# Kernel tuning notes

Hardware: AMD Instinct MI355X
Metric: run time of the kernel (lower is better)

## Reference

```python
import jax, jax.numpy as jnp
import numpy as np

# smoothing constants (from init_kwargs)
KERNEL_SIZE = 20
WINDOW = (-10.0, 10.0)
SIGMA = 4.0
AMPLITUDE = 0.5
N_SMOOTH = 331  # 350 - 20 + 1


def setup_inputs() -> dict:
    key = jax.random.key(0)
    ks = jax.random.split(key, 6)
    W, A, M, D = 4000, 64, 6, 500
    wavelengths = jnp.linspace(0.3, 2.5, W, dtype=jnp.float32)  # um
    grid = jnp.linspace(0.25, 2.6, D, dtype=jnp.float32)        # material wavelength tables
    n_tab = 1.3 + 1.5 * jax.random.uniform(ks[0], (M, D), dtype=jnp.float32)
    k_tab = 0.05 * jax.random.uniform(ks[1], (M, D), dtype=jnp.float32)
    fixed_data = jnp.stack([jnp.broadcast_to(grid, (M, D)), n_tab, k_tab], axis=1)  # [M,3,D]
    refractive_index = 1.5 + 1.5 * jax.random.uniform(ks[2], (350,), dtype=jnp.float32)
    compression_ratio = jnp.ones((1,), jnp.float32)
    thickness_above_unk = 0.05 + 0.2 * jax.random.uniform(ks[3], (10,), dtype=jnp.float32)  # um
    thickness_below_unk = 0.05 + 0.2 * jax.random.uniform(ks[4], (9,), dtype=jnp.float32)   # um
    angle_of_incidences = jnp.linspace(0.0, 60.0, A, dtype=jnp.float32)  # degrees
    # stack order: incoming | 10 above | unknown (index M) | 9 below | outgoing
    md = [0] + [1, 2] * 5 + [M] + [3, 4] * 4 + [3] + [5]
    material_distribution = jnp.array(md, dtype=jnp.int32)  # [22]
    unknown_layer_thickness = jnp.array([500.0], jnp.float32)  # nm
    return dict(refractive_index=refractive_index, compression_ratio=compression_ratio,
                fixed_data=fixed_data, thickness_above_unk=thickness_above_unk,
                thickness_below_unk=thickness_below_unk, wavelengths=wavelengths,
                angle_of_incidences=angle_of_incidences,
                material_distribution=material_distribution, polarization=0,
                unknown_layer_thickness=unknown_layer_thickness)


def reference(refractive_index, compression_ratio, fixed_data, thickness_above_unk,
              thickness_below_unk, wavelengths, angle_of_incidences,
              material_distribution, polarization, unknown_layer_thickness):
    D = fixed_data.shape[2]
    n_repeat = D - N_SMOOTH
    # --- gaussian smoothing of the unknown layer's refractive index (valid conv) ---
    x = jnp.linspace(WINDOW[0], WINDOW[1], KERNEL_SIZE)
    g = AMPLITUDE * jnp.exp(-0.5 * (x / SIGMA) ** 2)
    g = (g / jnp.sum(g)).astype(refractive_index.dtype)
    nk_s = jnp.convolve(refractive_index, g, mode='valid')            # [331]
    nk = jnp.concatenate([nk_s, jnp.full((n_repeat,), nk_s[-1], nk_s.dtype)])  # pad to max_data_dim
    dyn_wl = jnp.linspace(jnp.min(wavelengths), jnp.max(wavelengths), N_SMOOTH)
    dyn_wl = jnp.concatenate([dyn_wl, jnp.full((n_repeat,), dyn_wl[-1], dyn_wl.dtype)])
    # --- interpolate all material n,k tables onto the experimental wavelengths ---
    interp = jax.vmap(lambda xp, fp: jnp.interp(wavelengths, xp, fp))
    n_fixc = interp(fixed_data[:, 0], fixed_data[:, 1]) + 1j * interp(fixed_data[:, 0], fixed_data[:, 2])  # [M,W]
    n_unk = jnp.interp(wavelengths, dyn_wl, nk)[None].astype(n_fixc.dtype)  # unknown layer (k=0)
    n_mat = jnp.concatenate([n_fixc, n_unk], axis=0)                  # [M+1, W]
    n_stack = n_mat[material_distribution]                            # [Lyr, W] complex
    # --- thickness list (unknown in nm -> um, scaled by compression ratio) ---
    d_unk = unknown_layer_thickness / 1000.0 * compression_ratio      # [1]
    d = jnp.concatenate([thickness_above_unk, d_unk, thickness_below_unk])  # [L] = [20]
    # --- coherent TMM, vectorized over (angle, wavelength) ---
    th0 = jnp.deg2rad(angle_of_incidences)                            # [A]
    sin0 = (n_stack[0][None, :] * jnp.sin(th0)[:, None])              # [A,W] (Snell invariant)
    sin_th = sin0[None] / n_stack[:, None, :]                         # [Lyr,A,W]
    cos_th = jnp.sqrt(1.0 - sin_th ** 2)
    kz = 2.0 * jnp.pi * n_stack[:, None, :] * cos_th / wavelengths[None, None, :]
    delta = kz[1:-1] * d[:, None, None].astype(kz.dtype)              # [L,A,W]
    nc = n_stack[:, None, :]
    if polarization == 0:  # s-pol
        f = nc * cos_th                                               # [Lyr,A,W]
        r = (f[:-1] - f[1:]) / (f[:-1] + f[1:])                       # [L+1,A,W]
        t = 2.0 * f[:-1] / (f[:-1] + f[1:])
    else:  # p-pol
        num = nc[1:] * cos_th[:-1]
        den = nc[:-1] * cos_th[1:]
        r = (num - den) / (num + den)
        t = 2.0 * nc[:-1, ] * cos_th[:-1] / (num + den)
    # Mtilde = I_0 * prod_j (P_j @ I_j); 2x2 complex recursion via scan
    m00 = 1.0 / t[0]
    m01 = r[0] / t[0]
    m10 = m01
    m11 = m00

    def step(carry, xs):
        c00, c01, c10, c11 = carry
        dl, rj, tj = xs
        em = jnp.exp(-1j * dl) / tj
        ep = jnp.exp(1j * dl) / tj
        a, b, c, dd = em, rj * em, rj * ep, ep
        return (c00 * a + c01 * c, c00 * b + c01 * dd,
                c10 * a + c11 * c, c10 * b + c11 * dd), None

    (m00, m01, m10, m11), _ = jax.lax.scan(step, (m00, m01, m10, m11), (delta, r[1:], t[1:]))
    rr = m10 / m00
    tt = 1.0 / m00
    R = jnp.abs(rr) ** 2                                              # [A,W]
    if polarization == 0:
        f0 = n_stack[0][None] * cos_th[0]
        ff = n_stack[-1][None] * cos_th[-1]
        T = jnp.abs(tt) ** 2 * jnp.real(ff) / jnp.real(f0)
    else:
        T = (jnp.abs(tt) ** 2 * jnp.real(n_stack[-1][None] * jnp.conj(cos_th[-1]))
             / jnp.real(n_stack[0][None] * jnp.conj(cos_th[0])))
    Aabs = 1.0 - R - T
    return jnp.stack([R, T, Aabs])  # [3, A, W]
```

## Files before the change

kernel.cpp:

```cpp
#include <hip/hip_runtime.h>

#define DEV __device__ __forceinline__
#define RCP(x)  __builtin_amdgcn_rcpf(x)
#define SQRT(x) __builtin_amdgcn_sqrtf(x)

constexpr int W_  = 4000;
constexpr int A_  = 64;
constexpr int D_  = 500;
constexpr int NS_ = 331;
constexpr int KS_ = 20;
constexpr int L_  = 22;
constexpr float PIF = 3.14159265358979323846f;

struct cplx { float re, im; };

DEV cplx cmul(cplx a, cplx b) { return { a.re*b.re - a.im*b.im, a.re*b.im + a.im*b.re }; }
DEV cplx cinv(cplx z) {
  float d = RCP(fmaf(z.re, z.re, z.im * z.im));
  return { z.re * d, -z.im * d };
}

DEV cplx csqrtc(cplx z) {
  float x = z.re, y = z.im;
  float mag = SQRT(fmaf(x, x, y * y));
  float t   = SQRT(0.5f * (mag + fabsf(x)));
  float q   = y * 0.5f * RCP(t);
  bool pos  = (x >= 0.0f);
  float re  = pos ? t : fabsf(q);
  float im  = pos ? q : copysignf(t, y);
  return { re, im };
}

__global__ __launch_bounds__(256) void tmm_fused_kernel(
    const float* __restrict__ ri,
    const float* __restrict__ comp,
    const float* __restrict__ fixed,
    const float* __restrict__ tha,
    const float* __restrict__ thb,
    const float* __restrict__ wl,
    const float* __restrict__ ang,
    const int*   __restrict__ md,
    const float* __restrict__ unk,
    float* __restrict__ out)
{
  __shared__ float  s_grid[D_];
  __shared__ float  s_ri[350];
  __shared__ float  s_g[KS_];
  __shared__ int    s_md[L_];
  __shared__ float  s_d[20];
  __shared__ float  s_mn[4], s_mx[4];
  __shared__ float4 s_f[7 * 256];

  const int tid = threadIdx.x;

  for (int i = tid; i < D_;  i += 256) s_grid[i] = fixed[i];
  for (int i = tid; i < 350; i += 256) s_ri[i]   = ri[i];
  if (tid < KS_) {
    float x  = -10.0f + (float)tid * (20.0f / 19.0f);
    float xs = x * 0.25f;
    s_g[tid] = 0.5f * expf(-0.5f * xs * xs);
  }
  if (tid < L_) s_md[tid] = md[tid];
  if (tid < 20)
    s_d[tid] = (tid < 10) ? tha[tid]
             : (tid == 10 ? unk[0] / 1000.0f * comp[0] : thb[tid - 11]);

  float lmin = 3.4e38f, lmax = -3.4e38f;
  for (int i = tid; i < W_; i += 256) {
    float v = wl[i];
    lmin = fminf(lmin, v); lmax = fmaxf(lmax, v);
  }
  #pragma unroll
  for (int o = 32; o; o >>= 1) {
    lmin = fminf(lmin, __shfl_xor(lmin, o, 64));
    lmax = fmaxf(lmax, __shfl_xor(lmax, o, 64));
  }
  if ((tid & 63) == 0) { s_mn[tid >> 6] = lmin; s_mx[tid >> 6] = lmax; }
  __syncthreads();
  const float wmin = fminf(fminf(s_mn[0], s_mn[1]), fminf(s_mn[2], s_mn[3]));
  const float wmax = fmaxf(fmaxf(s_mx[0], s_mx[1]), fmaxf(s_mx[2], s_mx[3]));

  const int a  = blockIdx.y;
  const int w  = blockIdx.x * 256 + tid;
  const int wc = min(w, W_ - 1);
  const float x = wl[wc];

  int lo = 0, hi = D_;
  while (lo < hi) { int mid = (lo + hi) >> 1; if (s_grid[mid] <= x) lo = mid + 1; else hi = mid; }
  const int i = min(max(lo, 1), D_ - 1);
  const float gx0 = s_grid[i - 1];
  const float fr  = (x - gx0) * RCP(s_grid[i] - gx0);
  const bool lowc  = (x < s_grid[0]);
  const bool highc = (x > s_grid[D_ - 1]);

  #pragma unroll
  for (int m = 0; m < 6; ++m) {
    const float* nptr = fixed + (m * 3 + 1) * D_;
    const float* kptr = fixed + (m * 3 + 2) * D_;
    float nv = fmaf(fr, nptr[i] - nptr[i - 1], nptr[i - 1]);
    float kv = fmaf(fr, kptr[i] - kptr[i - 1], kptr[i - 1]);
    if (lowc)  { nv = nptr[0];      kv = kptr[0]; }
    if (highc) { nv = nptr[D_ - 1]; kv = kptr[D_ - 1]; }
    s_f[m * 256 + tid] = make_float4(nv, kv, 0.0f, 0.0f);
  }

  {
    float gsum = 0.0f;
    #pragma unroll
    for (int k = 0; k < KS_; ++k) gsum += s_g[k];
    const float ginv  = 1.0f / gsum;
    const float stepd = (wmax - wmin) / (float)(NS_ - 1);
    const float istep = RCP(stepd);
    int j = (int)floorf((x - wmin) * istep) + 1;
    j = min(max(j, 1), NS_ - 1);
    const int j0 = j - 1;
    float a0 = 0.0f, a1 = 0.0f;
    #pragma unroll
    for (int k = 0; k < KS_; ++k) {
      const float gk = s_g[KS_ - 1 - k];
      a0 = fmaf(s_ri[j0 + k], gk, a0);
      a1 = fmaf(s_ri[j0 + 1 + k], gk, a1);
    }
    a0 *= ginv; a1 *= ginv;
    const float d0 = fmaf((float)j0, stepd, wmin);
    const float d1 = fmaf((float)j,  stepd, wmin);
    const float f  = fmaf((x - d0) * RCP(d1 - d0), a1 - a0, a0);
    s_f[6 * 256 + tid] = make_float4(f, 0.0f, 0.0f, 0.0f);
  }

  const float th0  = ang[a] * (PIF / 180.0f);
  const float s0   = sinf(th0);
  const float klam = 2.0f * PIF * RCP(x);

  const int md0 = s_md[0];
  const float4 nn0 = s_f[md0 * 256 + tid];
  const cplx sin0 = { nn0.x * s0, nn0.y * s0 };

  #pragma unroll
  for (int m = 0; m < 7; ++m) {
    const float4 nn = s_f[m * 256 + tid];
    const cplx invn = cinv({ nn.x, nn.y });
    const cplx st   = cmul(sin0, invn);
    const cplx st2  = cmul(st, st);
    const cplx ct   = csqrtc({ 1.0f - st2.re, -st2.im });
    const cplx f    = cmul({ nn.x, nn.y }, ct);
    const cplx fi   = cinv(f);
    s_f[m * 256 + tid] = make_float4(f.re, f.im, fi.re, fi.im);
  }

  cplx u   = { 0.0f, 0.0f };
  cplx tac = { 1.0f, 0.0f };
  float4 fdn = s_f[s_md[L_ - 1] * 256 + tid];
  const float fL_re = fdn.x;

  #pragma unroll
  for (int j = L_ - 2; j >= 1; --j) {
    const float4 fj = s_f[s_md[j] * 256 + tid];
    const cplx q   = cmul({ fdn.x, fdn.y }, { fj.z, fj.w });
    const cplx iop = cinv({ 1.0f + q.re, q.im });
    const cplx r   = cmul({ 1.0f - q.re, -q.im }, iop);

    const float cst = klam * s_d[j - 1];
    const float dr = fj.x * cst, di = fj.y * cst;
    const float e2 = __expf(-di);
    float sn, cs;
    __sincosf(dr, &sn, &cs);
    const cplx ph   = { e2 * cs, e2 * sn };
    const cplx beta = cmul(ph, ph);

    const cplx ru  = cmul(r, u);
    const cplx idn = cinv({ 1.0f + ru.re, ru.im });
    tac = cmul(tac, cmul(cmul(iop, ph), idn));
    u = cmul(beta, cmul({ r.re + u.re, r.im + u.im }, idn));

    fdn = fj;
  }

  const float4 f0v = s_f[md0 * 256 + tid];
  const cplx q0   = cmul({ fdn.x, fdn.y }, { f0v.z, f0v.w });
  const cplx iop0 = cinv({ 1.0f + q0.re, q0.im });
  const cplx r0   = cmul({ 1.0f - q0.re, -q0.im }, iop0);
  const cplx ru0  = cmul(r0, u);
  const cplx idn0 = cinv({ 1.0f + ru0.re, ru0.im });
  const cplx rr   = cmul({ r0.re + u.re, r0.im + u.im }, idn0);
  cplx tt = cmul(cmul(iop0, idn0), tac);

  const float SC = 2097152.0f;
  tt.re *= SC; tt.im *= SC;

  const float R = fmaf(rr.re, rr.re, rr.im * rr.im);
  const float T = fmaf(tt.re, tt.re, tt.im * tt.im) * fL_re * RCP(f0v.x);

  if (w < W_) {
    const int o = a * W_ + w;
    out[o]               = R;
    out[A_ * W_ + o]     = T;
    out[2 * A_ * W_ + o] = 1.0f - R - T;
  }
}

extern "C" void kernel_launch(void* const* d_in, const int* in_sizes, int n_in,
                              void* d_out, int out_size, void* d_ws, size_t ws_size,
                              hipStream_t stream) {
  const float* ri    = (const float*)d_in[0];
  const float* comp  = (const float*)d_in[1];
  const float* fixed = (const float*)d_in[2];
  const float* tha   = (const float*)d_in[3];
  const float* thb   = (const float*)d_in[4];
  const float* wl    = (const float*)d_in[5];
  const float* ang   = (const float*)d_in[6];
  const int*   md    = (const int*)d_in[7];
  const float* unk   = (const float*)d_in[9];
  float* out = (float*)d_out;

  dim3 grid(16, A_);
  tmm_fused_kernel<<<grid, 256, 0, stream>>>(ri, comp, fixed, tha, thb, wl,
                                             ang, md, unk, out);
}
```

Before: 97.37 us.

## Split angle-independent material interpolation into a separate precompute kernel

Material interpolation, the Gaussian smoothing of the unknown index and the (n0/n_m)^2 ratio do not depend on angle, so they are moved into a small precompute kernel that runs once per wavelength and writes 7 float4 per wavelength to workspace. The main kernel then reads these values and only scales by sin^2 of the angle, which removes redundant interpolation, binary search and min/max reduction across all 64 angle blocks. The cost is a second launch with a serial dependency and extra global-memory traffic. The per-block shared-memory setup and the __syncthreads are also removed from the main kernel.

```diff
diff --git a/kernel.cpp b/kernel.cpp
--- a/kernel.cpp
+++ b/kernel.cpp
@@ -19,7 +19,6 @@
   float d = RCP(fmaf(z.re, z.re, z.im * z.im));
   return { z.re * d, -z.im * d };
 }
-
 DEV cplx csqrtc(cplx z) {
   float x = z.re, y = z.im;
   float mag = SQRT(fmaf(x, x, y * y));
@@ -31,25 +30,17 @@
   return { re, im };
 }
 
-__global__ __launch_bounds__(256) void tmm_fused_kernel(
+__global__ __launch_bounds__(256) void precompute_kernel(
     const float* __restrict__ ri,
-    const float* __restrict__ comp,
     const float* __restrict__ fixed,
-    const float* __restrict__ tha,
-    const float* __restrict__ thb,
     const float* __restrict__ wl,
-    const float* __restrict__ ang,
     const int*   __restrict__ md,
-    const float* __restrict__ unk,
-    float* __restrict__ out)
+    float4* __restrict__ nz)
 {
-  __shared__ float  s_grid[D_];
-  __shared__ float  s_ri[350];
-  __shared__ float  s_g[KS_];
-  __shared__ int    s_md[L_];
-  __shared__ float  s_d[20];
-  __shared__ float  s_mn[4], s_mx[4];
-  __shared__ float4 s_f[7 * 256];
+  __shared__ float s_grid[D_];
+  __shared__ float s_ri[350];
+  __shared__ float s_g[KS_];
+  __shared__ float s_mn[4], s_mx[4];
 
   const int tid = threadIdx.x;
 
@@ -60,10 +51,6 @@
     float xs = x * 0.25f;
     s_g[tid] = 0.5f * expf(-0.5f * xs * xs);
   }
-  if (tid < L_) s_md[tid] = md[tid];
-  if (tid < 20)
-    s_d[tid] = (tid < 10) ? tha[tid]
-             : (tid == 10 ? unk[0] / 1000.0f * comp[0] : thb[tid - 11]);
 
   float lmin = 3.4e38f, lmax = -3.4e38f;
   for (int i = tid; i < W_; i += 256) {
@@ -80,10 +67,11 @@
   const float wmin = fminf(fminf(s_mn[0], s_mn[1]), fminf(s_mn[2], s_mn[3]));
   const float wmax = fmaxf(fmaxf(s_mx[0], s_mx[1]), fmaxf(s_mx[2], s_mx[3]));
 
-  const int a  = blockIdx.y;
   const int w  = blockIdx.x * 256 + tid;
   const int wc = min(w, W_ - 1);
   const float x = wl[wc];
+
+  cplx nm[7];
 
   int lo = 0, hi = D_;
   while (lo < hi) { int mid = (lo + hi) >> 1; if (s_grid[mid] <= x) lo = mid + 1; else hi = mid; }
@@ -101,7 +89,7 @@
     float kv = fmaf(fr, kptr[i] - kptr[i - 1], kptr[i - 1]);
     if (lowc)  { nv = nptr[0];      kv = kptr[0]; }
     if (highc) { nv = nptr[D_ - 1]; kv = kptr[D_ - 1]; }
-    s_f[m * 256 + tid] = make_float4(nv, kv, 0.0f, 0.0f);
+    nm[m] = { nv, kv };
   }
 
   {
@@ -110,8 +98,7 @@
     for (int k = 0; k < KS_; ++k) gsum += s_g[k];
     const float ginv  = 1.0f / gsum;
     const float stepd = (wmax - wmin) / (float)(NS_ - 1);
-    const float istep = RCP(stepd);
-    int j = (int)floorf((x - wmin) * istep) + 1;
+    int j = (int)floorf((x - wmin) * RCP(stepd)) + 1;
     j = min(max(j, 1), NS_ - 1);
     const int j0 = j - 1;
     float a0 = 0.0f, a1 = 0.0f;
@@ -124,43 +111,73 @@
     a0 *= ginv; a1 *= ginv;
     const float d0 = fmaf((float)j0, stepd, wmin);
     const float d1 = fmaf((float)j,  stepd, wmin);
-    const float f  = fmaf((x - d0) * RCP(d1 - d0), a1 - a0, a0);
-    s_f[6 * 256 + tid] = make_float4(f, 0.0f, 0.0f, 0.0f);
-  }
+    nm[6] = { fmaf((x - d0) * RCP(d1 - d0), a1 - a0, a0), 0.0f };
+  }
+
+  const int m0 = md[0];
+  cplx n0 = nm[0];
+  #pragma unroll
+  for (int m = 1; m < 7; ++m) if (m0 == m) n0 = nm[m];
+
+  if (w < W_) {
+    #pragma unroll
+    for (int m = 0; m < 7; ++m) {
+      const cplx q = cmul(n0, cinv(nm[m]));
+      const cplx z = cmul(q, q);
+      nz[m * W_ + w] = make_float4(nm[m].re, nm[m].im, z.re, z.im);
+    }
+  }
+}
+
+__global__ __launch_bounds__(256) void tmm_kernel(
+    const float4* __restrict__ nz,
+    const float*  __restrict__ wl,
+    const float*  __restrict__ ang,
+    const int*    __restrict__ md,
+    const float*  __restrict__ tha,
+    const float*  __restrict__ thb,
+    const float*  __restrict__ unk,
+    const float*  __restrict__ comp,
+    float* __restrict__ out)
+{
+  __shared__ float4 s_f[7 * 256];
+
+  const int tid = threadIdx.x;
+  const int w = blockIdx.x * 256 + tid;
+  if (w >= W_) return;
+  const int a = blockIdx.y;
 
   const float th0  = ang[a] * (PIF / 180.0f);
   const float s0   = sinf(th0);
-  const float klam = 2.0f * PIF * RCP(x);
-
-  const int md0 = s_md[0];
-  const float4 nn0 = s_f[md0 * 256 + tid];
-  const cplx sin0 = { nn0.x * s0, nn0.y * s0 };
+  const float s0sq = s0 * s0;
+  const float klam = 2.0f * PIF * RCP(wl[w]);
 
   #pragma unroll
   for (int m = 0; m < 7; ++m) {
-    const float4 nn = s_f[m * 256 + tid];
-    const cplx invn = cinv({ nn.x, nn.y });
-    const cplx st   = cmul(sin0, invn);
-    const cplx st2  = cmul(st, st);
-    const cplx ct   = csqrtc({ 1.0f - st2.re, -st2.im });
-    const cplx f    = cmul({ nn.x, nn.y }, ct);
-    const cplx fi   = cinv(f);
+    const float4 v = nz[m * W_ + w];
+    const cplx st2 = { v.z * s0sq, v.w * s0sq };
+    const cplx ct  = csqrtc({ 1.0f - st2.re, -st2.im });
+    const cplx f   = cmul({ v.x, v.y }, ct);
+    const cplx fi  = cinv(f);
     s_f[m * 256 + tid] = make_float4(f.re, f.im, fi.re, fi.im);
   }
 
   cplx u   = { 0.0f, 0.0f };
   cplx tac = { 1.0f, 0.0f };
-  float4 fdn = s_f[s_md[L_ - 1] * 256 + tid];
+  float4 fdn = s_f[md[L_ - 1] * 256 + tid];
   const float fL_re = fdn.x;
 
   #pragma unroll
   for (int j = L_ - 2; j >= 1; --j) {
-    const float4 fj = s_f[s_md[j] * 256 + tid];
+    const float4 fj = s_f[md[j] * 256 + tid];
     const cplx q   = cmul({ fdn.x, fdn.y }, { fj.z, fj.w });
     const cplx iop = cinv({ 1.0f + q.re, q.im });
     const cplx r   = cmul({ 1.0f - q.re, -q.im }, iop);
 
-    const float cst = klam * s_d[j - 1];
+    const float dthj = (j - 1) < 10 ? tha[j - 1]
+                     : ((j - 1) == 10 ? unk[0] / 1000.0f * comp[0]
+                                      : thb[j - 12]);
+    const float cst = klam * dthj;
     const float dr = fj.x * cst, di = fj.y * cst;
     const float e2 = __expf(-di);
     float sn, cs;
@@ -176,7 +193,7 @@
     fdn = fj;
   }
 
-  const float4 f0v = s_f[md0 * 256 + tid];
+  const float4 f0v = s_f[md[0] * 256 + tid];
   const cplx q0   = cmul({ fdn.x, fdn.y }, { f0v.z, f0v.w });
   const cplx iop0 = cinv({ 1.0f + q0.re, q0.im });
   const cplx r0   = cmul({ 1.0f - q0.re, -q0.im }, iop0);
@@ -191,12 +208,10 @@
   const float R = fmaf(rr.re, rr.re, rr.im * rr.im);
   const float T = fmaf(tt.re, tt.re, tt.im * tt.im) * fL_re * RCP(f0v.x);
 
-  if (w < W_) {
-    const int o = a * W_ + w;
-    out[o]               = R;
-    out[A_ * W_ + o]     = T;
-    out[2 * A_ * W_ + o] = 1.0f - R - T;
-  }
+  const int o = a * W_ + w;
+  out[o]               = R;
+  out[A_ * W_ + o]     = T;
+  out[2 * A_ * W_ + o] = 1.0f - R - T;
 }
 
 extern "C" void kernel_launch(void* const* d_in, const int* in_sizes, int n_in,
@@ -213,7 +228,9 @@
   const float* unk   = (const float*)d_in[9];
   float* out = (float*)d_out;
 
+  float4* nz = (float4*)d_ws;
+
+  precompute_kernel<<<16, 256, 0, stream>>>(ri, fixed, wl, md, nz);
   dim3 grid(16, A_);
-  tmm_fused_kernel<<<grid, 256, 0, stream>>>(ri, comp, fixed, tha, thb, wl,
-                                             ang, md, unk, out);
-}
+  tmm_kernel<<<grid, 256, 0, stream>>>(nz, wl, ang, md, tha, thb, unk, comp, out);
+}
```

Measured after the change: 93.04 us. 1.05x faster.
